# Kernel tuning notes

Hardware: AMD Instinct MI355X
Metric: run time of the kernel (lower is better)

Reference implementation:

```python
import jax, jax.numpy as jnp
import numpy as np

NUM_STEPS = 8
ADD_IDENTITY = True
EPS = 1e-12
STANDARDIZE = True


def setup_inputs() -> dict:
    key = jax.random.key(0)
    N = 4096
    E = 65536  # avg degree 16
    edge_index = jax.random.randint(key, (2, E), 0, N, dtype=jnp.int64 if jax.config.jax_enable_x64 else jnp.int32)
    edge_weight = jnp.ones((E,), dtype=jnp.float32)
    return {"edge_index": edge_index, "edge_weight": edge_weight, "num_nodes": N}


def reference(edge_index, edge_weight, num_nodes):
    # A[i,j] = sum of edge_weight over edges (row=i, col=j); scipy sums duplicates,
    # and segment_sum does the same.
    row, col = edge_index[0], edge_index[1]
    # deg_j = column sums of A (A.sum(axis=0))
    deg = jax.ops.segment_sum(edge_weight, col, num_segments=num_nodes)
    deg = jnp.maximum(deg, EPS)
    # M = A @ D^{-1}:  M[row, col] = w / deg[col]
    w = edge_weight / deg[col]  # [E]

    # Carry dense propagator P = M^t, extract diagonals for t = 1..NUM_STEPS.
    P0 = jnp.eye(num_nodes, dtype=jnp.float32)  # [N, N]

    def step(P, _):
        # P_new[i, :] = sum_{edges (i=row, j=col)} w_e * P[j, :]
        P = jax.ops.segment_sum(w[:, None] * P[col], row, num_segments=num_nodes)
        return P, jnp.diagonal(P)

    _, diags = jax.lax.scan(step, P0, None, length=NUM_STEPS)  # [T, N]

    X = diags.T  # [N, T]
    if ADD_IDENTITY:
        X = jnp.concatenate([jnp.ones((num_nodes, 1), dtype=jnp.float32), X], axis=1)
    if STANDARDIZE:
        mean = X.mean(axis=0, keepdims=True)
        std = jnp.maximum(X.std(axis=0, keepdims=True), 1e-6)  # ddof=0 == unbiased=False
        X = (X - mean) / std
    return X
```

## Files before the change

kernel.cpp:

```cpp
#include <hip/hip_runtime.h>

#define NN 4096
#define TSTEPS 8
#define EPSW 1e-12f
#define SLABW 512
#define NSLAB 8
#define LSLAB 9
#define BUCKET 64
#define LBUCK 6
#define SLAB_ELEMS ((size_t)NN * SLABW)

typedef unsigned int uint32;
typedef uint32 uint4v __attribute__((ext_vector_type(4)));
typedef float f32x2 __attribute__((ext_vector_type(2)));

__device__ __forceinline__ uint32 bf16rn(float f) {
  uint32 b = __float_as_uint(f);
  return (b + 0x7FFFu + ((b >> 16) & 1u)) >> 16;
}
__device__ __forceinline__ float bf2f(ushort u) {
  return __uint_as_float(((uint32)u) << 16);
}
__device__ __forceinline__ float rdlanef(float v, int k) {
  return __uint_as_float(__builtin_amdgcn_readlane(__float_as_uint(v), k));
}
__device__ __forceinline__ int sphys(int c) {
  int blk = c >> 3;
  return ((blk ^ ((blk >> 3) & 7)) << 3) | (c & 7);
}

__global__ __launch_bounds__(256) void deg_kernel(
    const int* __restrict__ cols, const float* __restrict__ ew,
    float* __restrict__ deg, int E) {
  int e = blockIdx.x * 256 + threadIdx.x;
  if (e >= E) return;
  atomicAdd(deg + cols[e], ew[e]);
}

__global__ __launch_bounds__(256) void scatter_kernel(
    const int* __restrict__ rows, const int* __restrict__ cols,
    const float* __restrict__ ew, const float* __restrict__ deg,
    int* __restrict__ fill, int* __restrict__ col_s, float* __restrict__ w_s,
    float* __restrict__ diags, int E) {
  int e = blockIdx.x * 256 + threadIdx.x;
  if (e >= E) return;
  int r = rows[e], c = cols[e];
  float w = ew[e] / fmaxf(deg[c], EPSW);
  int pos = atomicAdd(fill + r, 1);
  if (pos < BUCKET) {
    col_s[(r << LBUCK) + pos] = c;
    w_s[(r << LBUCK) + pos] = w;
  }
  if (r == c) atomicAdd(diags + r, w);
}

__global__ __launch_bounds__(64) void m2_csr_kernel(
    const int* __restrict__ fill, const int* __restrict__ col_s,
    const float* __restrict__ w_s, ushort* __restrict__ dst,
    float* __restrict__ diags) {
  int i = blockIdx.x;
  int tid = threadIdx.x;
  __shared__ float acc[NN];
  float4 z4 = make_float4(0.f, 0.f, 0.f, 0.f);
#pragma unroll
  for (int k = 0; k < 16; ++k) *(float4*)(acc + k * 256 + tid * 4) = z4;
  int cnt = min(fill[i], BUCKET);
  __syncthreads();
  int myc = 0;
  float myw = 0.f;
  if (tid < cnt) {
    myc = col_s[(i << LBUCK) + tid];
    myw = w_s[(i << LBUCK) + tid];
  }
  for (int e = 0; e < cnt; ++e) {
    int j = __builtin_amdgcn_readlane(myc, e);
    float we = rdlanef(myw, e);
    int fcnt = min(fill[j], BUCKET);
    if (tid < fcnt)
      atomicAdd(acc + sphys(col_s[(j << LBUCK) + tid]),
                we * w_s[(j << LBUCK) + tid]);
  }
  __syncthreads();
  if (tid == 0) diags[NN + i] = acc[sphys(i)];
#pragma unroll
  for (int p = 0; p < 8; ++p) {
    int c = p * SLABW + tid * 8;
    int ph = sphys(c);
    float4 lo = *(const float4*)(acc + ph);
    float4 hi = *(const float4*)(acc + ph + 4);
    uint4v o;
    o.x = bf16rn(lo.x) | (bf16rn(lo.y) << 16);
    o.y = bf16rn(lo.z) | (bf16rn(lo.w) << 16);
    o.z = bf16rn(hi.x) | (bf16rn(hi.y) << 16);
    o.w = bf16rn(hi.z) | (bf16rn(hi.w) << 16);
    *(uint4v*)(dst + (size_t)p * SLAB_ELEMS + (size_t)i * SLABW + tid * 8) = o;
  }
}

#define FMA8(u, wv)                                          \
  do {                                                       \
    f32x2 w2_ = {(wv), (wv)};                                \
    _Pragma("unroll") for (int q = 0; q < 4; ++q) {          \
      f32x2 p_;                                              \
      p_.x = __uint_as_float((u)[q] << 16);                  \
      p_.y = __uint_as_float((u)[q] & 0xFFFF0000u);          \
      acc2[q] = p_ * w2_ + acc2[q];                          \
    }                                                        \
  } while (0)

__global__ __launch_bounds__(256) void spmm_kernel(
    const ushort* __restrict__ src, ushort* __restrict__ dst,
    const int* __restrict__ fill, const int* __restrict__ col_s,
    const float* __restrict__ w_s, float* __restrict__ diags, int tIdx) {
  int b = blockIdx.x;
  int slab = b & (NSLAB - 1);
  int wv = threadIdx.x >> 6;
  int lane = threadIdx.x & 63;
  int i = ((b >> 3) << 2) | wv;
  int cnt = min(fill[i], BUCKET);
  __shared__ int sc_all[4][64];
  __shared__ float sw_all[4][64];
  int* sc = sc_all[wv];
  float* sw = sw_all[wv];
  f32x2 acc2[4];
#pragma unroll
  for (int q = 0; q < 4; ++q) acc2[q] = (f32x2){0.f, 0.f};
  const ushort* sbase = src + (size_t)slab * SLAB_ELEMS + lane * 8;

  if (lane < cnt) {
    sc[lane] = col_s[(i << LBUCK) + lane];
    sw[lane] = w_s[(i << LBUCK) + lane];
  }
  int k = 0;
  for (; k + 8 <= cnt; k += 8) {
    uint4v u0 = *(const uint4v*)(sbase + ((size_t)sc[k]     << LSLAB));
    uint4v u1 = *(const uint4v*)(sbase + ((size_t)sc[k + 1] << LSLAB));
    uint4v u2 = *(const uint4v*)(sbase + ((size_t)sc[k + 2] << LSLAB));
    uint4v u3 = *(const uint4v*)(sbase + ((size_t)sc[k + 3] << LSLAB));
    uint4v u4 = *(const uint4v*)(sbase + ((size_t)sc[k + 4] << LSLAB));
    uint4v u5 = *(const uint4v*)(sbase + ((size_t)sc[k + 5] << LSLAB));
    uint4v u6 = *(const uint4v*)(sbase + ((size_t)sc[k + 6] << LSLAB));
    uint4v u7 = *(const uint4v*)(sbase + ((size_t)sc[k + 7] << LSLAB));
    float w0 = sw[k], w1 = sw[k + 1], w2 = sw[k + 2], w3 = sw[k + 3];
    float w4 = sw[k + 4], w5 = sw[k + 5], w6 = sw[k + 6], w7 = sw[k + 7];
    FMA8(u0, w0); FMA8(u1, w1); FMA8(u2, w2); FMA8(u3, w3);
    FMA8(u4, w4); FMA8(u5, w5); FMA8(u6, w6); FMA8(u7, w7);
  }
  for (; k + 4 <= cnt; k += 4) {
    uint4v u0 = *(const uint4v*)(sbase + ((size_t)sc[k]     << LSLAB));
    uint4v u1 = *(const uint4v*)(sbase + ((size_t)sc[k + 1] << LSLAB));
    uint4v u2 = *(const uint4v*)(sbase + ((size_t)sc[k + 2] << LSLAB));
    uint4v u3 = *(const uint4v*)(sbase + ((size_t)sc[k + 3] << LSLAB));
    float w0 = sw[k], w1 = sw[k + 1], w2 = sw[k + 2], w3 = sw[k + 3];
    FMA8(u0, w0); FMA8(u1, w1); FMA8(u2, w2); FMA8(u3, w3);
  }
  for (; k < cnt; ++k) {
    uint4v u = *(const uint4v*)(sbase + ((size_t)sc[k] << LSLAB));
    float w = sw[k];
    FMA8(u, w);
  }

  uint4v o;
#pragma unroll
  for (int q = 0; q < 4; ++q)
    o[q] = bf16rn(acc2[q].x) | (bf16rn(acc2[q].y) << 16);
  *(uint4v*)(dst + (size_t)slab * SLAB_ELEMS + (size_t)i * SLABW + lane * 8) = o;

  if ((i >> LSLAB) == slab) {
    int lc = i & (SLABW - 1);
    if ((lc >> 3) == lane) {
      int m = lc & 7;
      f32x2 pr = acc2[m >> 1];
      float v = (m & 1) ? pr.y : pr.x;
      diags[tIdx * NN + i] = v;
    }
  }
}

__device__ __forceinline__ size_t slab_addr(int row, int col) {
  return ((size_t)(col >> LSLAB)) * SLAB_ELEMS + (size_t)row * SLABW + (col & (SLABW - 1));
}
__device__ __forceinline__ float elem8(uint4v lo, uint4v hi, int c) {
  uint32 u = (c < 8) ? lo[(c & 7) >> 1] : hi[(c & 7) >> 1];
  return __uint_as_float((c & 1) ? (u & 0xFFFF0000u) : (u << 16));
}

__global__ __launch_bounds__(256) void trace_kernel(
    const ushort* __restrict__ M2, const ushort* __restrict__ M3,
    const ushort* __restrict__ M4, float* __restrict__ diags) {
  int bid = blockIdx.x;
  int bi = bid >> 3, jc = bid & 7;
  int tid = threadIdx.x;
  __shared__ ushort b3[64 * 64], b4[64 * 64];
  __shared__ float red[4][4][64];
  int lr = tid >> 2, lc0 = (tid & 3) * 16;
  int r = tid & 63, jq = tid >> 6;
  float s5 = 0.f, s6 = 0.f, s7 = 0.f, s8 = 0.f;

  for (int it = 0; it < 8; ++it) {
    int bj = jc * 8 + it;
    {
      int gj = bj * 64 + lr;
      int gc = bi * 64 + lc0;
      size_t base = slab_addr(gj, gc);
      uint4v v3a = *(const uint4v*)(M3 + base);
      uint4v v3b = *(const uint4v*)(M3 + base + 8);
      uint4v v4a = *(const uint4v*)(M4 + base);
      uint4v v4b = *(const uint4v*)(M4 + base + 8);
      int cb0 = (lc0 >> 3) ^ (lr & 7);
      int cb1 = ((lc0 >> 3) + 1) ^ (lr & 7);
      *(uint4v*)(b3 + lr * 64 + cb0 * 8) = v3a;
      *(uint4v*)(b3 + lr * 64 + cb1 * 8) = v3b;
      *(uint4v*)(b4 + lr * 64 + cb0 * 8) = v4a;
      *(uint4v*)(b4 + lr * 64 + cb1 * 8) = v4b;
    }
    __syncthreads();
    int gi = bi * 64 + r;
    int gc0 = bj * 64 + jq * 16;
    size_t abase = slab_addr(gi, gc0);
    uint4v a2a = *(const uint4v*)(M2 + abase);
    uint4v a2b = *(const uint4v*)(M2 + abase + 8);
    uint4v a3a = *(const uint4v*)(M3 + abase);
    uint4v a3b = *(const uint4v*)(M3 + abase + 8);
    uint4v a4a = *(const uint4v*)(M4 + abase);
    uint4v a4b = *(const uint4v*)(M4 + abase + 8);
#pragma unroll
    for (int c = 0; c < 16; ++c) {
      int jj = jq * 16 + c;
      int idx = jj * 64 + ((((r >> 3) ^ (jj & 7)) << 3) | (r & 7));
      float bv3 = bf2f(b3[idx]);
      float bv4 = bf2f(b4[idx]);
      float av2 = elem8(a2a, a2b, c);
      float av3 = elem8(a3a, a3b, c);
      float av4 = elem8(a4a, a4b, c);
      s5 += av2 * bv3;
      s6 += av3 * bv3;
      s7 += av3 * bv4;
      s8 += av4 * bv4;
    }
    __syncthreads();
  }
  red[0][jq][r] = s5;
  red[1][jq][r] = s6;
  red[2][jq][r] = s7;
  red[3][jq][r] = s8;
  __syncthreads();
  if (tid < 64) {
    int gi = bi * 64 + tid;
#pragma unroll
    for (int v = 0; v < 4; ++v) {
      float s = red[v][0][tid] + red[v][1][tid] + red[v][2][tid] + red[v][3][tid];
      atomicAdd(diags + (4 + v) * NN + gi, s);
    }
  }
}

__global__ __launch_bounds__(256) void finalize_kernel(const float* __restrict__ diags,
                                                       float* __restrict__ out) {
  int k = blockIdx.x;
  int tid = threadIdx.x;
  float vals[16];
  float sum = 0.f, sq = 0.f;
#pragma unroll
  for (int j = 0; j < 16; ++j) {
    int i = j * 256 + tid;
    float v = (k == 0) ? 1.0f : diags[(k - 1) * NN + i];
    vals[j] = v;
    sum += v;
    sq += v * v;
  }
#pragma unroll
  for (int off = 32; off; off >>= 1) {
    sum += __shfl_down(sum, off);
    sq += __shfl_down(sq, off);
  }
  __shared__ float s0[4], s1[4];
  __shared__ float smean, sinv;
  int wid = tid >> 6, lane = tid & 63;
  if (lane == 0) { s0[wid] = sum; s1[wid] = sq; }
  __syncthreads();
  if (tid == 0) {
    float S = s0[0] + s0[1] + s0[2] + s0[3];
    float Q = s1[0] + s1[1] + s1[2] + s1[3];
    float mean = S / (float)NN;
    float var = Q / (float)NN - mean * mean;
    var = fmaxf(var, 0.f);
    float sd = fmaxf(sqrtf(var), 1e-6f);
    smean = mean;
    sinv = 1.f / sd;
  }
  __syncthreads();
#pragma unroll
  for (int j = 0; j < 16; ++j) {
    int i = j * 256 + tid;
    out[i * (TSTEPS + 1) + k] = (vals[j] - smean) * sinv;
  }
}

extern "C" void kernel_launch(void* const* d_in, const int* in_sizes, int n_in,
                              void* d_out, int out_size, void* d_ws, size_t ws_size,
                              hipStream_t stream) {
  const int* ei = (const int*)d_in[0];
  const float* ew = (const float*)d_in[1];
  int E = in_sizes[1];
  const int* rows = ei;
  const int* cols = ei + E;

  char* ws = (char*)d_ws;
  size_t off = 0;
  auto alloc = [&](size_t bytes) {
    void* p = ws + off;
    off = (off + bytes + 255) & ~(size_t)255;
    return p;
  };
  float* deg   = (float*)alloc(NN * 4);
  int*   fill  = (int*)alloc(NN * 4);
  float* diags = (float*)alloc((size_t)TSTEPS * NN * 4);
  size_t zbytes = off;
  int*   col_s = (int*)alloc((size_t)NN * BUCKET * 4);
  float* w_s   = (float*)alloc((size_t)NN * BUCKET * 4);
  ushort* bufA = (ushort*)alloc((size_t)NN * NN * 2);
  ushort* bufB = (ushort*)alloc((size_t)NN * NN * 2);
  ushort* bufC = (ushort*)alloc((size_t)NN * NN * 2);

  hipMemsetAsync(deg, 0, zbytes, stream);

  int eb = (E + 255) / 256;
  deg_kernel<<<eb, 256, 0, stream>>>(cols, ew, deg, E);
  scatter_kernel<<<eb, 256, 0, stream>>>(rows, cols, ew, deg, fill, col_s, w_s,
                                         diags, E);

  m2_csr_kernel<<<NN, 64, 0, stream>>>(fill, col_s, w_s, bufA, diags);
  spmm_kernel<<<(NN / 4) * NSLAB, 256, 0, stream>>>(bufA, bufB, fill, col_s, w_s, diags, 2);
  spmm_kernel<<<(NN / 4) * NSLAB, 256, 0, stream>>>(bufB, bufC, fill, col_s, w_s, diags, 3);
  trace_kernel<<<512, 256, 0, stream>>>(bufA, bufB, bufC, diags);

  finalize_kernel<<<TSTEPS + 1, 256, 0, stream>>>(diags, (float*)d_out);
}
```

Measured before the change: 133.0 us.

## Parallelize M2 neighbor expansion, deepen SpMM unroll, replace trace atomics with partials

```diff
diff --git a/kernel.cpp b/kernel.cpp
--- a/kernel.cpp
+++ b/kernel.cpp
@@ -21,9 +21,6 @@
 __device__ __forceinline__ float bf2f(ushort u) {
   return __uint_as_float(((uint32)u) << 16);
 }
-__device__ __forceinline__ float rdlanef(float v, int k) {
-  return __uint_as_float(__builtin_amdgcn_readlane(__float_as_uint(v), k));
-}
 __device__ __forceinline__ int sphys(int c) {
   int blk = c >> 3;
   return ((blk ^ ((blk >> 3) & 7)) << 3) | (c & 7);
@@ -41,7 +38,7 @@
     const int* __restrict__ rows, const int* __restrict__ cols,
     const float* __restrict__ ew, const float* __restrict__ deg,
     int* __restrict__ fill, int* __restrict__ col_s, float* __restrict__ w_s,
-    float* __restrict__ diags, int E) {
+    int E) {
   int e = blockIdx.x * 256 + threadIdx.x;
   if (e >= E) return;
   int r = rows[e], c = cols[e];
@@ -51,7 +48,6 @@
     col_s[(r << LBUCK) + pos] = c;
     w_s[(r << LBUCK) + pos] = w;
   }
-  if (r == c) atomicAdd(diags + r, w);
 }
 
 __global__ __launch_bounds__(64) void m2_csr_kernel(
@@ -66,19 +62,31 @@
   for (int k = 0; k < 16; ++k) *(float4*)(acc + k * 256 + tid * 4) = z4;
   int cnt = min(fill[i], BUCKET);
   __syncthreads();
-  int myc = 0;
+  int myc = 0, fj = 0;
   float myw = 0.f;
   if (tid < cnt) {
     myc = col_s[(i << LBUCK) + tid];
     myw = w_s[(i << LBUCK) + tid];
-  }
-  for (int e = 0; e < cnt; ++e) {
-    int j = __builtin_amdgcn_readlane(myc, e);
-    float we = rdlanef(myw, e);
-    int fcnt = min(fill[j], BUCKET);
-    if (tid < fcnt)
-      atomicAdd(acc + sphys(col_s[(j << LBUCK) + tid]),
-                we * w_s[(j << LBUCK) + tid]);
+    fj = min(fill[myc], BUCKET);
+  }
+  float sl = (tid < cnt && myc == i) ? myw : 0.f;
+#pragma unroll
+  for (int o = 32; o; o >>= 1) sl += __shfl_down(sl, o);
+  if (tid == 0) diags[i] = sl;
+
+  int g = tid >> 4, f0 = tid & 15;
+  for (int e = 0; e < cnt; e += 4) {
+    int idx = e + g;
+    bool v = idx < cnt;
+    int srcl = v ? idx : 0;
+    int j = __shfl(myc, srcl);
+    float we = __shfl(myw, srcl);
+    int fc = __shfl(fj, srcl);
+    if (v) {
+      for (int f = f0; f < fc; f += 16)
+        atomicAdd(acc + sphys(col_s[(j << LBUCK) + f]),
+                  we * w_s[(j << LBUCK) + f]);
+    }
   }
   __syncthreads();
   if (tid == 0) diags[NN + i] = acc[sphys(i)];
@@ -132,27 +140,35 @@
     sw[lane] = w_s[(i << LBUCK) + lane];
   }
   int k = 0;
+  for (; k + 16 <= cnt; k += 16) {
+    uint4v u[16];
+    float wl[16];
+#pragma unroll
+    for (int t = 0; t < 16; ++t) u[t] = *(const uint4v*)(sbase + ((size_t)sc[k + t] << LSLAB));
+#pragma unroll
+    for (int t = 0; t < 16; ++t) wl[t] = sw[k + t];
+#pragma unroll
+    for (int t = 0; t < 16; ++t) FMA8(u[t], wl[t]);
+  }
   for (; k + 8 <= cnt; k += 8) {
-    uint4v u0 = *(const uint4v*)(sbase + ((size_t)sc[k]     << LSLAB));
-    uint4v u1 = *(const uint4v*)(sbase + ((size_t)sc[k + 1] << LSLAB));
-    uint4v u2 = *(const uint4v*)(sbase + ((size_t)sc[k + 2] << LSLAB));
-    uint4v u3 = *(const uint4v*)(sbase + ((size_t)sc[k + 3] << LSLAB));
-    uint4v u4 = *(const uint4v*)(sbase + ((size_t)sc[k + 4] << LSLAB));
-    uint4v u5 = *(const uint4v*)(sbase + ((size_t)sc[k + 5] << LSLAB));
-    uint4v u6 = *(const uint4v*)(sbase + ((size_t)sc[k + 6] << LSLAB));
-    uint4v u7 = *(const uint4v*)(sbase + ((size_t)sc[k + 7] << LSLAB));
-    float w0 = sw[k], w1 = sw[k + 1], w2 = sw[k + 2], w3 = sw[k + 3];
-    float w4 = sw[k + 4], w5 = sw[k + 5], w6 = sw[k + 6], w7 = sw[k + 7];
-    FMA8(u0, w0); FMA8(u1, w1); FMA8(u2, w2); FMA8(u3, w3);
-    FMA8(u4, w4); FMA8(u5, w5); FMA8(u6, w6); FMA8(u7, w7);
+    uint4v u[8];
+    float wl[8];
+#pragma unroll
+    for (int t = 0; t < 8; ++t) u[t] = *(const uint4v*)(sbase + ((size_t)sc[k + t] << LSLAB));
+#pragma unroll
+    for (int t = 0; t < 8; ++t) wl[t] = sw[k + t];
+#pragma unroll
+    for (int t = 0; t < 8; ++t) FMA8(u[t], wl[t]);
   }
   for (; k + 4 <= cnt; k += 4) {
-    uint4v u0 = *(const uint4v*)(sbase + ((size_t)sc[k]     << LSLAB));
-    uint4v u1 = *(const uint4v*)(sbase + ((size_t)sc[k + 1] << LSLAB));
-    uint4v u2 = *(const uint4v*)(sbase + ((size_t)sc[k + 2] << LSLAB));
-    uint4v u3 = *(const uint4v*)(sbase + ((size_t)sc[k + 3] << LSLAB));
-    float w0 = sw[k], w1 = sw[k + 1], w2 = sw[k + 2], w3 = sw[k + 3];
-    FMA8(u0, w0); FMA8(u1, w1); FMA8(u2, w2); FMA8(u3, w3);
+    uint4v u[4];
+    float wl[4];
+#pragma unroll
+    for (int t = 0; t < 4; ++t) u[t] = *(const uint4v*)(sbase + ((size_t)sc[k + t] << LSLAB));
+#pragma unroll
+    for (int t = 0; t < 4; ++t) wl[t] = sw[k + t];
+#pragma unroll
+    for (int t = 0; t < 4; ++t) FMA8(u[t], wl[t]);
   }
   for (; k < cnt; ++k) {
     uint4v u = *(const uint4v*)(sbase + ((size_t)sc[k] << LSLAB));
@@ -187,7 +203,7 @@
 
 __global__ __launch_bounds__(256) void trace_kernel(
     const ushort* __restrict__ M2, const ushort* __restrict__ M3,
-    const ushort* __restrict__ M4, float* __restrict__ diags) {
+    const ushort* __restrict__ M4, float* __restrict__ part) {
   int bid = blockIdx.x;
   int bi = bid >> 3, jc = bid & 7;
   int tid = threadIdx.x;
@@ -250,13 +266,14 @@
 #pragma unroll
     for (int v = 0; v < 4; ++v) {
       float s = red[v][0][tid] + red[v][1][tid] + red[v][2][tid] + red[v][3][tid];
-      atomicAdd(diags + (4 + v) * NN + gi, s);
-    }
-  }
-}
-
-__global__ __launch_bounds__(256) void finalize_kernel(const float* __restrict__ diags,
-                                                       float* __restrict__ out) {
+      part[((size_t)v * 8 + jc) * NN + gi] = s;
+    }
+  }
+}
+
+__global__ __launch_bounds__(256) void finalize_kernel(
+    const float* __restrict__ diags, const float* __restrict__ part,
+    float* __restrict__ out) {
   int k = blockIdx.x;
   int tid = threadIdx.x;
   float vals[16];
@@ -264,7 +281,17 @@
 #pragma unroll
   for (int j = 0; j < 16; ++j) {
     int i = j * 256 + tid;
-    float v = (k == 0) ? 1.0f : diags[(k - 1) * NN + i];
+    float v;
+    if (k == 0) {
+      v = 1.0f;
+    } else if (k <= 4) {
+      v = diags[(size_t)(k - 1) * NN + i];
+    } else {
+      v = 0.f;
+      const float* p = part + (size_t)(k - 5) * 8 * NN + i;
+#pragma unroll
+      for (int jc = 0; jc < 8; ++jc) v += p[(size_t)jc * NN];
+    }
     vals[j] = v;
     sum += v;
     sq += v * v;
@@ -315,8 +342,9 @@
   };
   float* deg   = (float*)alloc(NN * 4);
   int*   fill  = (int*)alloc(NN * 4);
-  float* diags = (float*)alloc((size_t)TSTEPS * NN * 4);
   size_t zbytes = off;
+  float* diags = (float*)alloc((size_t)4 * NN * 4);
+  float* part  = (float*)alloc((size_t)4 * 8 * NN * 4);
   int*   col_s = (int*)alloc((size_t)NN * BUCKET * 4);
   float* w_s   = (float*)alloc((size_t)NN * BUCKET * 4);
   ushort* bufA = (ushort*)alloc((size_t)NN * NN * 2);
@@ -327,13 +355,12 @@
 
   int eb = (E + 255) / 256;
   deg_kernel<<<eb, 256, 0, stream>>>(cols, ew, deg, E);
-  scatter_kernel<<<eb, 256, 0, stream>>>(rows, cols, ew, deg, fill, col_s, w_s,
-                                         diags, E);
+  scatter_kernel<<<eb, 256, 0, stream>>>(rows, cols, ew, deg, fill, col_s, w_s, E);
 
   m2_csr_kernel<<<NN, 64, 0, stream>>>(fill, col_s, w_s, bufA, diags);
   spmm_kernel<<<(NN / 4) * NSLAB, 256, 0, stream>>>(bufA, bufB, fill, col_s, w_s, diags, 2);
   spmm_kernel<<<(NN / 4) * NSLAB, 256, 0, stream>>>(bufB, bufC, fill, col_s, w_s, diags, 3);
-  trace_kernel<<<512, 256, 0, stream>>>(bufA, bufB, bufC, diags);
-
-  finalize_kernel<<<TSTEPS + 1, 256, 0, stream>>>(diags, (float*)d_out);
-}
+  trace_kernel<<<512, 256, 0, stream>>>(bufA, bufB, bufC, part);
+
+  finalize_kernel<<<TSTEPS + 1, 256, 0, stream>>>(diags, part, (float*)d_out);
+}
```

New measurement: 145.9 us. 1.1x slower.
